# Kernel optimization log

Hardware: AMD Instinct MI355X
Metric: run time of the kernel (lower is better)

## Reference

```python
import jax, jax.numpy as jnp
import numpy as np

B, S, C, H, W = 8, 32, 3, 256, 256


def setup_inputs() -> dict:
    key = jax.random.key(0)
    k1, k2 = jax.random.split(key)
    return {
        "input": jax.random.normal(k1, (B, S, C, H, W), dtype=jnp.float32),
        "target": jax.random.normal(k2, (B, C, H, W), dtype=jnp.float32),
    }


def _l2norm(x, axis):
    # F.normalize: x / max(||x||_2, eps)
    return x / jnp.maximum(jnp.linalg.norm(x, axis=axis, keepdims=True), 1e-12)


def _forward(input, target):
    b, s, c, h, w = input.shape
    # target: [B,C,H,W] -> permute(0,1,3,2) -> [B,C,W,H] -> flatten(1,2) -> [B, C*W, H]
    target_f = _l2norm(jnp.transpose(target, (0, 1, 3, 2)).reshape(b, c * w, h), axis=1)
    # input: [B,S,C,H,W] -> permute(0,1,2,4,3) -> [B,S,C,W,H] -> flatten(2,3) -> [B,S,C*W,H]
    input_f = _l2norm(jnp.transpose(input, (0, 1, 2, 4, 3)).reshape(b, s, c * w, h), axis=2)

    def corr_one(xf, wf):
        # xf: [S, C*W, H] as conv batch, wf: [C*W, H] as single-output-channel kernel
        y = jax.lax.conv_general_dilated(
            xf, wf[None], window_strides=(1,), padding=[(h - 1, h - 1)],
            dimension_numbers=("NCH", "OIH", "NCH"))
        return y[:, 0, :h]  # first H shift positions (overlap sizes 1..H)

    corr = jax.vmap(corr_one)(input_f, target_f)  # [B, S, H]
    corr = corr / jnp.arange(1, h + 1, dtype=input.dtype)  # mean over overlap size

    overlap = jnp.argmax(corr, axis=-1)            # [B, S] best overlap per sample
    shift = (h - 1) - overlap                      # rows to shift up by

    # out[b,s,:,r,:] = input[b,s,:,r+shift,:] for r < overlap, else 0
    h_idx = jnp.arange(h)[None, None, :] + shift[:, :, None]  # [B, S, H]
    valid = h_idx < h
    idx = jnp.clip(h_idx, 0, h - 1)[:, :, None, :, None]      # [B,S,1,H,1]
    gathered = jnp.take_along_axis(input, idx, axis=3)
    return jnp.where(valid[:, :, None, :, None], gathered, jnp.zeros((), input.dtype))


def reference(input, target):
    return _forward(input, target)
```

## Files before the change

### kernel.cpp

```cpp
#include <hip/hip_runtime.h>

#define B_ 8
#define S_ 32
#define C_ 3
#define H_ 256
#define W_ 256
#define HW_ (H_*W_)
#define CHW_ (C_*H_*W_)
#define NT_ 24
#define TILE_ELEMS 8192

typedef __attribute__((ext_vector_type(8))) short bf16x8;
typedef __attribute__((ext_vector_type(4))) float f32x4;
typedef unsigned int u32;
typedef u32 __attribute__((address_space(3)))* lds_u32p;
typedef const u32 __attribute__((address_space(1)))* glb_u32p;

__device__ __forceinline__ void split2(float x, float y, unsigned &hp, unsigned &lp) {
  unsigned ux = __float_as_uint(x), uy = __float_as_uint(y);
  unsigned hx = ux & 0xFFFF0000u, hy = uy & 0xFFFF0000u;
  float lx = x - __uint_as_float(hx);
  float ly = y - __uint_as_float(hy);
  hp = (ux >> 16) | hy;
  lp = (__float_as_uint(lx) >> 16) | (__float_as_uint(ly) & 0xFFFF0000u);
}

__device__ __forceinline__ void gl2lds16(const ushort* g, ushort* l) {
  __builtin_amdgcn_global_load_lds((glb_u32p)g, (lds_u32p)l, 16, 0, 0);
}

__global__ void ct_ntg(const float* __restrict__ target, float* __restrict__ rntg) {
  int r = (int)((blockIdx.x * (size_t)blockDim.x + threadIdx.x) >> 6);
  int lane = threadIdx.x & 63;
  const float* base = target + (size_t)(r >> 8) * CHW_ + (size_t)(r & 255) * W_;
  float ss = 0.f;
#pragma unroll
  for (int c = 0; c < C_; ++c)
#pragma unroll
    for (int tt = 0; tt < W_/64; ++tt) {
      float v = base[c*HW_ + tt*64 + lane];
      ss = fmaf(v, v, ss);
    }
#pragma unroll
  for (int off = 32; off; off >>= 1) ss += __shfl_xor(ss, off);
  if (lane == 0) rntg[r] = 1.0f / fmaxf(sqrtf(ss), 1e-12f);
}

__global__ void ct_bsplit(const float* __restrict__ target,
                          ushort* __restrict__ BhG, ushort* __restrict__ BlG) {
  int bx = blockIdx.x;
  int b  = bx / 24, kt = bx % 24;
  int c  = kt >> 3, w0 = (kt & 7) * 32;
  int t  = threadIdx.x;
  int trow = t >> 3, tw = t & 7;
  const float* base = target + (size_t)(b*C_ + c) * HW_ + w0 + tw*4;
  ushort* oh = BhG + (size_t)bx * TILE_ELEMS;
  ushort* ol = BlG + (size_t)bx * TILE_ELEMS;
#pragma unroll
  for (int i = 0; i < 8; ++i) {
    int row = trow + 32*i;
    float4 v = *(const float4*)(base + (size_t)row * W_);
    unsigned h0, l0, h1, l1;
    split2(v.x, v.y, h0, l0); split2(v.z, v.w, h1, l1);
    int idx = (row>>4)*512 + (tw>>1)*128 + (row&15)*8 + (tw&1)*4;
    *(uint2*)&oh[idx] = make_uint2(h0, h1);
    *(uint2*)&ol[idx] = make_uint2(l0, l1);
  }
}

__global__ __launch_bounds__(512)
void ct_corr_mfma(const float* __restrict__ input,
                  const ushort* __restrict__ BhG, const ushort* __restrict__ BlG,
                  const float* __restrict__ rntg_g,
                  int* __restrict__ shift_out) {
  __shared__ ushort AhL[8192], AlL[8192], BhL[8192], BlL[8192];
  __shared__ float ninSq[256], rnin[256], rntg_s[256], corrS[256];
  __shared__ unsigned long long wkey[4];

  const int bs = blockIdx.x;
  const int bG = bs >> 5;
  const int t  = threadIdx.x;
  const int lane = t & 63;
  const int wid  = t >> 6;
  const int wm   = wid >> 2;
  const int wn   = wid & 3;

  const float* Abase = input + (size_t)bs * CHW_;

  if (t < 256) { ninSq[t] = 0.f; corrS[t] = 0.f; rntg_s[t] = rntg_g[bG*256 + t]; }

  f32x4 acc[8][4];
#pragma unroll
  for (int m = 0; m < 8; ++m)
#pragma unroll
    for (int n = 0; n < 4; ++n) acc[m][n] = (f32x4){0.f, 0.f, 0.f, 0.f};

  float4 pa[4];
  float ssA[4] = {0.f, 0.f, 0.f, 0.f};

  auto issueA = [&](int kt) {
    const float* Ab = Abase + (size_t)(kt >> 3) * HW_ + (kt & 7) * 32;
#pragma unroll
    for (int p = 0; p < 4; ++p) {
      int f   = p * 512 + t;
      int row = (f >> 7) * 16 + ((f >> 1) & 15);
      int kk  = ((f >> 5) & 3) * 8 + (f & 1) * 4;
      pa[p] = *(const float4*)(Ab + (size_t)row * W_ + kk);
    }
  };

  auto stashA = [&]() {
#pragma unroll
    for (int p = 0; p < 4; ++p) {
      int f   = p * 512 + t;
      int idx = (f >> 7) * 512 + ((f >> 5) & 3) * 128 + ((f >> 1) & 15) * 8 + (f & 1) * 4;
      float4 va = pa[p];
      ssA[p] = fmaf(va.x, va.x, fmaf(va.y, va.y,
               fmaf(va.z, va.z, fmaf(va.w, va.w, ssA[p]))));
      unsigned h0, l0, h1, l1;
      split2(va.x, va.y, h0, l0); split2(va.z, va.w, h1, l1);
      *(uint2*)&AhL[idx] = make_uint2(h0, h1);
      *(uint2*)&AlL[idx] = make_uint2(l0, l1);
    }
  };

  issueA(0);

  for (int kt = 0; kt < NT_; ++kt) {
    __syncthreads();
    if (wid < 4) {
      const ushort* gh = BhG + (size_t)(bG*NT_ + kt) * TILE_ELEMS + wid*2048;
      const ushort* gl = BlG + (size_t)(bG*NT_ + kt) * TILE_ELEMS + wid*2048;
#pragma unroll
      for (int o = 0; o < 4; ++o)
        gl2lds16(gh + o*512 + lane*8, &BhL[wid*2048 + o*512]);
#pragma unroll
      for (int o = 0; o < 4; ++o)
        gl2lds16(gl + o*512 + lane*8, &BlL[wid*2048 + o*512]);
    }
    stashA();
    __syncthreads();
    if (kt < NT_ - 1) issueA(kt + 1);

    bf16x8 bh[4], bl[4];
#pragma unroll
    for (int n = 0; n < 4; ++n) {
      int ct = wn * 4 + n;
      bh[n] = *(const bf16x8*)&BhL[ct * 512 + lane * 8];
      bl[n] = *(const bf16x8*)&BlL[ct * 512 + lane * 8];
    }
#pragma unroll
    for (int m = 0; m < 8; ++m) {
      int rt = wm * 8 + m;
      bf16x8 ah = *(const bf16x8*)&AhL[rt * 512 + lane * 8];
      bf16x8 al = *(const bf16x8*)&AlL[rt * 512 + lane * 8];
#pragma unroll
      for (int n = 0; n < 4; ++n) {
        acc[m][n] = __builtin_amdgcn_mfma_f32_16x16x32_bf16(ah, bh[n], acc[m][n], 0, 0, 0);
        acc[m][n] = __builtin_amdgcn_mfma_f32_16x16x32_bf16(ah, bl[n], acc[m][n], 0, 0, 0);
        acc[m][n] = __builtin_amdgcn_mfma_f32_16x16x32_bf16(al, bh[n], acc[m][n], 0, 0, 0);
      }
    }
  }

#pragma unroll
  for (int p = 0; p < 4; ++p) {
    int f = p * 512 + t;
    int row = (f >> 7) * 16 + ((f >> 1) & 15);
    atomicAdd(&ninSq[row], ssA[p]);
  }
  __syncthreads();
  if (t < 256) rnin[t] = 1.0f / fmaxf(sqrtf(ninSq[t]), 1e-12f);
  __syncthreads();

#pragma unroll
  for (int n = 0; n < 4; ++n) {
    int col = wn*64 + n*16 + (lane & 15);
    float rc = rntg_s[col];
#pragma unroll
    for (int m = 0; m < 8; ++m) {
      f32x4 a = acc[m][n];
#pragma unroll
      for (int r = 0; r < 4; ++r) {
        int row = wm*128 + m*16 + (lane >> 4)*4 + r;
        int q = col - row;
        if (q >= 0) atomicAdd(&corrS[q], a[r] * rnin[row] * rc);
      }
    }
  }
  __syncthreads();

  if (t < 256) {
    int q = 255 - t;
    float v = corrS[q] / (float)(256 - q);
    unsigned u = __float_as_uint(v);
    u = (u & 0x80000000u) ? ~u : (u | 0x80000000u);
    unsigned long long key = ((unsigned long long)u << 32) | (unsigned)q;
#pragma unroll
    for (int off = 32; off; off >>= 1) {
      unsigned long long o = __shfl_xor(key, off);
      if (o > key) key = o;
    }
    if ((t & 63) == 0) wkey[t >> 6] = key;
  }
  __syncthreads();
  if (t == 0) {
    unsigned long long k = wkey[0];
#pragma unroll
    for (int i = 1; i < 4; ++i) if (wkey[i] > k) k = wkey[i];
    shift_out[bs] = (int)(k & 0xFFFFFFFFull);
  }
}

__global__ void ct_gather(const float* __restrict__ input,
                          const int* __restrict__ shift,
                          float* __restrict__ out) {
  size_t idx = (size_t)blockIdx.x * blockDim.x + threadIdx.x;
  int w4 = (int)(idx & 63);
  int h  = (int)((idx >> 6) & 255);
  int sc = (int)(idx >> 14);
  int bs = sc / 3;
  int hh = h + shift[bs];
  float4 v = make_float4(0.f, 0.f, 0.f, 0.f);
  if (hh < H_) v = *(const float4*)(input + ((size_t)sc << 16) + (size_t)hh * W_ + w4*4);
  *(float4*)(out + (idx << 2)) = v;
}

extern "C" void kernel_launch(void* const* d_in, const int* in_sizes, int n_in,
                              void* d_out, int out_size, void* d_ws, size_t ws_size,
                              hipStream_t stream) {
  const float* input  = (const float*)d_in[0];
  const float* target = (const float*)d_in[1];
  float* out = (float*)d_out;

  float* rntg  = (float*)d_ws;
  int*   shift = (int*)(rntg + 2048);
  ushort* BhG  = (ushort*)(shift + 256);
  ushort* BlG  = BhG + (size_t)B_ * NT_ * TILE_ELEMS;

  ct_ntg       <<<512, 256, 0, stream>>>(target, rntg);
  ct_bsplit    <<<B_ * NT_, 256, 0, stream>>>(target, BhG, BlG);
  ct_corr_mfma <<<B_ * S_, 512, 0, stream>>>(input, BhG, BlG, rntg, shift);
  ct_gather    <<<(B_*S_*C_*H_*W_/4) / 256, 256, 0, stream>>>(input, shift, out);
}
```

Baseline: 173.3 us.

## Load B fragments straight into registers with double buffering, widen A stash

The B operand tiles are no longer staged through LDS with global_load_lds. Each wave now loads its B fragments directly from global memory into registers, double-buffered across even and odd k-tiles so the next tile's loads overlap the current MFMAs. The A load mapping is changed so each thread loads two adjacent float4s and writes 16-byte LDS stores, and the row-norm partials shrink to two per thread. This frees half of the LDS and removes the B LDS round trip, at the cost of more VGPRs, which may lower occupancy, and of redundant B global loads across the waves that share a column group.

```diff
diff --git a/kernel.cpp b/kernel.cpp
--- a/kernel.cpp
+++ b/kernel.cpp
@@ -12,9 +12,6 @@
 
 typedef __attribute__((ext_vector_type(8))) short bf16x8;
 typedef __attribute__((ext_vector_type(4))) float f32x4;
-typedef unsigned int u32;
-typedef u32 __attribute__((address_space(3)))* lds_u32p;
-typedef const u32 __attribute__((address_space(1)))* glb_u32p;
 
 __device__ __forceinline__ void split2(float x, float y, unsigned &hp, unsigned &lp) {
   unsigned ux = __float_as_uint(x), uy = __float_as_uint(y);
@@ -23,10 +20,6 @@
   float ly = y - __uint_as_float(hy);
   hp = (ux >> 16) | hy;
   lp = (__float_as_uint(lx) >> 16) | (__float_as_uint(ly) & 0xFFFF0000u);
-}
-
-__device__ __forceinline__ void gl2lds16(const ushort* g, ushort* l) {
-  __builtin_amdgcn_global_load_lds((glb_u32p)g, (lds_u32p)l, 16, 0, 0);
 }
 
 __global__ void ct_ntg(const float* __restrict__ target, float* __restrict__ rntg) {
@@ -73,7 +66,7 @@
                   const ushort* __restrict__ BhG, const ushort* __restrict__ BlG,
                   const float* __restrict__ rntg_g,
                   int* __restrict__ shift_out) {
-  __shared__ ushort AhL[8192], AlL[8192], BhL[8192], BlL[8192];
+  __shared__ ushort AhL[8192], AlL[8192];
   __shared__ float ninSq[256], rnin[256], rntg_s[256], corrS[256];
   __shared__ unsigned long long wkey[4];
 
@@ -95,80 +88,80 @@
 #pragma unroll
     for (int n = 0; n < 4; ++n) acc[m][n] = (f32x4){0.f, 0.f, 0.f, 0.f};
 
+  const int row0 = ((t >> 6) & 7) * 16 + (t & 15);
+  const int kcol = ((t >> 4) & 3) * 8;
   float4 pa[4];
-  float ssA[4] = {0.f, 0.f, 0.f, 0.f};
+  float ssA[2] = {0.f, 0.f};
+  bf16x8 bhE[4], blE[4], bhO[4], blO[4];
 
   auto issueA = [&](int kt) {
-    const float* Ab = Abase + (size_t)(kt >> 3) * HW_ + (kt & 7) * 32;
-#pragma unroll
-    for (int p = 0; p < 4; ++p) {
-      int f   = p * 512 + t;
-      int row = (f >> 7) * 16 + ((f >> 1) & 15);
-      int kk  = ((f >> 5) & 3) * 8 + (f & 1) * 4;
-      pa[p] = *(const float4*)(Ab + (size_t)row * W_ + kk);
-    }
+    const float* Ab = Abase + (size_t)(kt >> 3) * HW_ + (kt & 7) * 32 + kcol;
+    pa[0] = *(const float4*)(Ab + (size_t)row0 * W_);
+    pa[1] = *(const float4*)(Ab + (size_t)row0 * W_ + 4);
+    pa[2] = *(const float4*)(Ab + (size_t)(row0 + 128) * W_);
+    pa[3] = *(const float4*)(Ab + (size_t)(row0 + 128) * W_ + 4);
   };
 
   auto stashA = [&]() {
 #pragma unroll
-    for (int p = 0; p < 4; ++p) {
-      int f   = p * 512 + t;
-      int idx = (f >> 7) * 512 + ((f >> 5) & 3) * 128 + ((f >> 1) & 15) * 8 + (f & 1) * 4;
-      float4 va = pa[p];
-      ssA[p] = fmaf(va.x, va.x, fmaf(va.y, va.y,
-               fmaf(va.z, va.z, fmaf(va.w, va.w, ssA[p]))));
-      unsigned h0, l0, h1, l1;
-      split2(va.x, va.y, h0, l0); split2(va.z, va.w, h1, l1);
-      *(uint2*)&AhL[idx] = make_uint2(h0, h1);
-      *(uint2*)&AlL[idx] = make_uint2(l0, l1);
+    for (int g = 0; g < 2; ++g) {
+      float4 a = pa[2*g], b = pa[2*g + 1];
+      ssA[g] = fmaf(a.x, a.x, fmaf(a.y, a.y, fmaf(a.z, a.z, fmaf(a.w, a.w,
+               fmaf(b.x, b.x, fmaf(b.y, b.y, fmaf(b.z, b.z, fmaf(b.w, b.w, ssA[g]))))))));
+      uint4 hu, lu;
+      split2(a.x, a.y, hu.x, lu.x); split2(a.z, a.w, hu.y, lu.y);
+      split2(b.x, b.y, hu.z, lu.z); split2(b.z, b.w, hu.w, lu.w);
+      int go = (t + g*512) * 8;
+      *(uint4*)&AhL[go] = hu;
+      *(uint4*)&AlL[go] = lu;
     }
   };
 
+#define ISSUE_B(KT, BH, BL) {                                                 \
+    const ushort* gh = BhG + (size_t)(bG*NT_ + (KT)) * TILE_ELEMS + wn*2048 + lane*8; \
+    const ushort* gl = BlG + (size_t)(bG*NT_ + (KT)) * TILE_ELEMS + wn*2048 + lane*8; \
+    _Pragma("unroll")                                                         \
+    for (int n = 0; n < 4; ++n) {                                             \
+      BH[n] = *(const bf16x8*)(gh + n*512);                                   \
+      BL[n] = *(const bf16x8*)(gl + n*512);                                   \
+    } }
+
+#define MFMA_BODY(BH, BL) {                                                   \
+    _Pragma("unroll")                                                         \
+    for (int m = 0; m < 8; ++m) {                                             \
+      int rt = wm*8 + m;                                                      \
+      bf16x8 ah = *(const bf16x8*)&AhL[rt*512 + lane*8];                      \
+      bf16x8 al = *(const bf16x8*)&AlL[rt*512 + lane*8];                      \
+      _Pragma("unroll")                                                       \
+      for (int n = 0; n < 4; ++n) {                                           \
+        acc[m][n] = __builtin_amdgcn_mfma_f32_16x16x32_bf16(ah, BH[n], acc[m][n], 0, 0, 0); \
+        acc[m][n] = __builtin_amdgcn_mfma_f32_16x16x32_bf16(ah, BL[n], acc[m][n], 0, 0, 0); \
+        acc[m][n] = __builtin_amdgcn_mfma_f32_16x16x32_bf16(al, BH[n], acc[m][n], 0, 0, 0); \
+      } } }
+
   issueA(0);
-
-  for (int kt = 0; kt < NT_; ++kt) {
-    __syncthreads();
-    if (wid < 4) {
-      const ushort* gh = BhG + (size_t)(bG*NT_ + kt) * TILE_ELEMS + wid*2048;
-      const ushort* gl = BlG + (size_t)(bG*NT_ + kt) * TILE_ELEMS + wid*2048;
-#pragma unroll
-      for (int o = 0; o < 4; ++o)
-        gl2lds16(gh + o*512 + lane*8, &BhL[wid*2048 + o*512]);
-#pragma unroll
-      for (int o = 0; o < 4; ++o)
-        gl2lds16(gl + o*512 + lane*8, &BlL[wid*2048 + o*512]);
-    }
+  ISSUE_B(0, bhE, blE);
+
+  for (int it = 0; it < 12; ++it) {
+    const int k0 = 2*it;
+    __syncthreads();
     stashA();
     __syncthreads();
-    if (kt < NT_ - 1) issueA(kt + 1);
-
-    bf16x8 bh[4], bl[4];
-#pragma unroll
-    for (int n = 0; n < 4; ++n) {
-      int ct = wn * 4 + n;
-      bh[n] = *(const bf16x8*)&BhL[ct * 512 + lane * 8];
-      bl[n] = *(const bf16x8*)&BlL[ct * 512 + lane * 8];
-    }
-#pragma unroll
-    for (int m = 0; m < 8; ++m) {
-      int rt = wm * 8 + m;
-      bf16x8 ah = *(const bf16x8*)&AhL[rt * 512 + lane * 8];
-      bf16x8 al = *(const bf16x8*)&AlL[rt * 512 + lane * 8];
-#pragma unroll
-      for (int n = 0; n < 4; ++n) {
-        acc[m][n] = __builtin_amdgcn_mfma_f32_16x16x32_bf16(ah, bh[n], acc[m][n], 0, 0, 0);
-        acc[m][n] = __builtin_amdgcn_mfma_f32_16x16x32_bf16(ah, bl[n], acc[m][n], 0, 0, 0);
-        acc[m][n] = __builtin_amdgcn_mfma_f32_16x16x32_bf16(al, bh[n], acc[m][n], 0, 0, 0);
-      }
-    }
-  }
-
-#pragma unroll
-  for (int p = 0; p < 4; ++p) {
-    int f = p * 512 + t;
-    int row = (f >> 7) * 16 + ((f >> 1) & 15);
-    atomicAdd(&ninSq[row], ssA[p]);
-  }
+    issueA(k0 + 1);
+    ISSUE_B(k0 + 1, bhO, blO);
+    MFMA_BODY(bhE, blE);
+    __syncthreads();
+    stashA();
+    __syncthreads();
+    if (it < 11) {
+      issueA(k0 + 2);
+      ISSUE_B(k0 + 2, bhE, blE);
+    }
+    MFMA_BODY(bhO, blO);
+  }
+
+  atomicAdd(&ninSq[row0], ssA[0]);
+  atomicAdd(&ninSq[row0 + 128], ssA[1]);
   __syncthreads();
   if (t < 256) rnin[t] = 1.0f / fmaxf(sqrtf(ninSq[t]), 1e-12f);
   __syncthreads();
```

New measurement: 185.2 us. +6.9%, slower.

## Load MFMA operands directly from global memory, dropping LDS staging

Applied to the files above, without the earlier changes.

The correlation kernel no longer stages the A (input) and B (target split) tiles in shared memory. Each wave now loads its own A rows as fp32 straight from global memory, splits them into bf16 hi/lo in registers, and reads the B fragments directly from the pre-split global buffers. This removes the per-K-tile barriers and the LDS write/read traffic. In exchange, each A element is loaded four times (once per wn wave), B is re-read by every wm wave, and the software prefetch of the next tile is gone, so the kernel relies on cache hits and latency hiding.

```diff
diff --git a/kernel.cpp b/kernel.cpp
--- a/kernel.cpp
+++ b/kernel.cpp
@@ -12,9 +12,6 @@
 
 typedef __attribute__((ext_vector_type(8))) short bf16x8;
 typedef __attribute__((ext_vector_type(4))) float f32x4;
-typedef unsigned int u32;
-typedef u32 __attribute__((address_space(3)))* lds_u32p;
-typedef const u32 __attribute__((address_space(1)))* glb_u32p;
 
 __device__ __forceinline__ void split2(float x, float y, unsigned &hp, unsigned &lp) {
   unsigned ux = __float_as_uint(x), uy = __float_as_uint(y);
@@ -23,10 +20,6 @@
   float ly = y - __uint_as_float(hy);
   hp = (ux >> 16) | hy;
   lp = (__float_as_uint(lx) >> 16) | (__float_as_uint(ly) & 0xFFFF0000u);
-}
-
-__device__ __forceinline__ void gl2lds16(const ushort* g, ushort* l) {
-  __builtin_amdgcn_global_load_lds((glb_u32p)g, (lds_u32p)l, 16, 0, 0);
 }
 
 __global__ void ct_ntg(const float* __restrict__ target, float* __restrict__ rntg) {
@@ -73,7 +66,6 @@
                   const ushort* __restrict__ BhG, const ushort* __restrict__ BlG,
                   const float* __restrict__ rntg_g,
                   int* __restrict__ shift_out) {
-  __shared__ ushort AhL[8192], AlL[8192], BhL[8192], BlL[8192];
   __shared__ float ninSq[256], rnin[256], rntg_s[256], corrS[256];
   __shared__ unsigned long long wkey[4];
 
@@ -84,10 +76,11 @@
   const int wid  = t >> 6;
   const int wm   = wid >> 2;
   const int wn   = wid & 3;
-
-  const float* Abase = input + (size_t)bs * CHW_;
+  const int lr   = lane & 15;
+  const int kg   = lane >> 4;
 
   if (t < 256) { ninSq[t] = 0.f; corrS[t] = 0.f; rntg_s[t] = rntg_g[bG*256 + t]; }
+  __syncthreads();
 
   f32x4 acc[8][4];
 #pragma unroll
@@ -95,65 +88,32 @@
 #pragma unroll
     for (int n = 0; n < 4; ++n) acc[m][n] = (f32x4){0.f, 0.f, 0.f, 0.f};
 
-  float4 pa[4];
-  float ssA[4] = {0.f, 0.f, 0.f, 0.f};
-
-  auto issueA = [&](int kt) {
-    const float* Ab = Abase + (size_t)(kt >> 3) * HW_ + (kt & 7) * 32;
-#pragma unroll
-    for (int p = 0; p < 4; ++p) {
-      int f   = p * 512 + t;
-      int row = (f >> 7) * 16 + ((f >> 1) & 15);
-      int kk  = ((f >> 5) & 3) * 8 + (f & 1) * 4;
-      pa[p] = *(const float4*)(Ab + (size_t)row * W_ + kk);
-    }
-  };
-
-  auto stashA = [&]() {
-#pragma unroll
-    for (int p = 0; p < 4; ++p) {
-      int f   = p * 512 + t;
-      int idx = (f >> 7) * 512 + ((f >> 5) & 3) * 128 + ((f >> 1) & 15) * 8 + (f & 1) * 4;
-      float4 va = pa[p];
-      ssA[p] = fmaf(va.x, va.x, fmaf(va.y, va.y,
-               fmaf(va.z, va.z, fmaf(va.w, va.w, ssA[p]))));
-      unsigned h0, l0, h1, l1;
-      split2(va.x, va.y, h0, l0); split2(va.z, va.w, h1, l1);
-      *(uint2*)&AhL[idx] = make_uint2(h0, h1);
-      *(uint2*)&AlL[idx] = make_uint2(l0, l1);
-    }
-  };
-
-  issueA(0);
+  float ssA[8] = {0.f,0.f,0.f,0.f,0.f,0.f,0.f,0.f};
+
+  const float* Arow = input + (size_t)bs * CHW_ + (size_t)(wm*128 + lr) * W_ + kg*8;
 
   for (int kt = 0; kt < NT_; ++kt) {
-    __syncthreads();
-    if (wid < 4) {
-      const ushort* gh = BhG + (size_t)(bG*NT_ + kt) * TILE_ELEMS + wid*2048;
-      const ushort* gl = BlG + (size_t)(bG*NT_ + kt) * TILE_ELEMS + wid*2048;
-#pragma unroll
-      for (int o = 0; o < 4; ++o)
-        gl2lds16(gh + o*512 + lane*8, &BhL[wid*2048 + o*512]);
-#pragma unroll
-      for (int o = 0; o < 4; ++o)
-        gl2lds16(gl + o*512 + lane*8, &BlL[wid*2048 + o*512]);
-    }
-    stashA();
-    __syncthreads();
-    if (kt < NT_ - 1) issueA(kt + 1);
-
+    const ushort* gh = BhG + (size_t)(bG*NT_ + kt) * TILE_ELEMS + wn*2048 + lane*8;
+    const ushort* gl = BlG + (size_t)(bG*NT_ + kt) * TILE_ELEMS + wn*2048 + lane*8;
     bf16x8 bh[4], bl[4];
 #pragma unroll
     for (int n = 0; n < 4; ++n) {
-      int ct = wn * 4 + n;
-      bh[n] = *(const bf16x8*)&BhL[ct * 512 + lane * 8];
-      bl[n] = *(const bf16x8*)&BlL[ct * 512 + lane * 8];
-    }
+      bh[n] = *(const bf16x8*)(gh + n*512);
+      bl[n] = *(const bf16x8*)(gl + n*512);
+    }
+    const float* Ab = Arow + (size_t)(kt >> 3) * HW_ + (kt & 7) * 32;
 #pragma unroll
     for (int m = 0; m < 8; ++m) {
-      int rt = wm * 8 + m;
-      bf16x8 ah = *(const bf16x8*)&AhL[rt * 512 + lane * 8];
-      bf16x8 al = *(const bf16x8*)&AlL[rt * 512 + lane * 8];
+      float4 a0 = *(const float4*)(Ab + (size_t)m * 16 * W_);
+      float4 a1 = *(const float4*)(Ab + (size_t)m * 16 * W_ + 4);
+      if (wn == 0)
+        ssA[m] = fmaf(a0.x, a0.x, fmaf(a0.y, a0.y, fmaf(a0.z, a0.z, fmaf(a0.w, a0.w,
+                 fmaf(a1.x, a1.x, fmaf(a1.y, a1.y, fmaf(a1.z, a1.z, fmaf(a1.w, a1.w, ssA[m]))))))));
+      uint4 hu, lu;
+      split2(a0.x, a0.y, hu.x, lu.x); split2(a0.z, a0.w, hu.y, lu.y);
+      split2(a1.x, a1.y, hu.z, lu.z); split2(a1.z, a1.w, hu.w, lu.w);
+      bf16x8 ah = __builtin_bit_cast(bf16x8, hu);
+      bf16x8 al = __builtin_bit_cast(bf16x8, lu);
 #pragma unroll
       for (int n = 0; n < 4; ++n) {
         acc[m][n] = __builtin_amdgcn_mfma_f32_16x16x32_bf16(ah, bh[n], acc[m][n], 0, 0, 0);
@@ -163,11 +123,10 @@
     }
   }
 
-#pragma unroll
-  for (int p = 0; p < 4; ++p) {
-    int f = p * 512 + t;
-    int row = (f >> 7) * 16 + ((f >> 1) & 15);
-    atomicAdd(&ninSq[row], ssA[p]);
+  if (wn == 0) {
+#pragma unroll
+    for (int m = 0; m < 8; ++m)
+      atomicAdd(&ninSq[wm*128 + m*16 + lr], ssA[m]);
   }
   __syncthreads();
   if (t < 256) rnin[t] = 1.0f / fmaxf(sqrtf(ninSq[t]), 1e-12f);
@@ -175,14 +134,14 @@
 
 #pragma unroll
   for (int n = 0; n < 4; ++n) {
-    int col = wn*64 + n*16 + (lane & 15);
+    int col = wn*64 + n*16 + lr;
     float rc = rntg_s[col];
 #pragma unroll
     for (int m = 0; m < 8; ++m) {
       f32x4 a = acc[m][n];
 #pragma unroll
       for (int r = 0; r < 4; ++r) {
-        int row = wm*128 + m*16 + (lane >> 4)*4 + r;
+        int row = wm*128 + m*16 + kg*4 + r;
         int q = col - row;
         if (q >= 0) atomicAdd(&corrS[q], a[r] * rnin[row] * rc);
       }
```

Result: slower. 234.8 us (+35.5%).
